# Kernel optimization log

Hardware: AMD Instinct MI355X
Metric: run time of the kernel (lower is better)

Reference implementation:

```python
import jax, jax.numpy as jnp
import numpy as np

D_CAT = 4096   # number of multinomial categories (input_dim)
HID = 256      # hidden_dim
B = 4096       # batch_size (eta is a (B, D_CAT-1) parameter)
INIT = 1e-3
LOG2PI = float(np.log(2.0 * np.pi))


def _helmert_basis(d):
    """Orthonormal ILR balance basis, shape (d-1, d): rows sum to 0, Psi @ Psi.T = I."""
    i = np.arange(1, d, dtype=np.float64)
    scale = np.sqrt(i / (i + 1.0))
    Psi = np.zeros((d - 1, d), dtype=np.float64)
    tri = np.tril(np.ones((d - 1, d - 1), dtype=np.float64))
    Psi[:, : d - 1] = tri * (scale / i)[:, None]
    Psi[np.arange(d - 1), np.arange(1, d)] = -scale
    return Psi.astype(np.float32)


def setup_inputs() -> dict:
    key = jax.random.key(0)
    k1, k2, k3, k4 = jax.random.split(key, 4)
    n = D_CAT - 1
    x = jax.random.randint(k1, (B, D_CAT), 0, 20).astype(jnp.float32)  # count data
    Psi = jnp.asarray(_helmert_basis(D_CAT))                            # (n, D)
    enc_W = jax.random.normal(k2, (HID, n), dtype=jnp.float32) * INIT   # encoder Linear weight
    dec_W = jax.random.normal(k3, (n, HID), dtype=jnp.float32) * INIT   # decoder Linear weight
    variational_logvars = jnp.zeros((HID,), jnp.float32)
    log_sigma_sq = jnp.float32(0.01)
    eta = jax.random.normal(k4, (B, n), dtype=jnp.float32) * INIT       # learned eta parameter
    return dict(x=x, Psi=Psi, enc_W=enc_W, dec_W=dec_W,
                variational_logvars=variational_logvars,
                log_sigma_sq=log_sigma_sq, eta=eta)


def reference(x, Psi, enc_W, dec_W, variational_logvars, log_sigma_sq, eta):
    # --- ILR transform of imputed counts: clr(log(x+1)) @ Psi^T ---
    logp = jnp.log(x + 1.0)                                   # imputer: x + 1
    clr = logp - logp.mean(-1, keepdims=True)                 # (B, D)
    hx = clr @ Psi.T                                          # (B, n)
    z_mean = hx @ enc_W.T                                     # (B, k)
    mu = z_mean @ dec_W.T                                     # (B, n)

    # --- MultivariateNormalFactorIdentity log_prob via Woodbury / det lemma ---
    # Sigma = var * I_n + W diag(Dv) W^T,  W = dec_W (n, k)
    Dv = jnp.exp(variational_logvars)                         # (k,)
    var = jnp.exp(log_sigma_sq)                               # scalar
    n = dec_W.shape[0]
    WtW = dec_W.T @ dec_W                                     # (k, k)
    M = jnp.diag(1.0 / Dv) + WtW / var                        # capacitance matrix (k, k)
    d = eta - mu                                              # (B, n)
    dW = d @ dec_W                                            # (B, k)
    sol = jnp.linalg.solve(M, dW.T).T                         # (B, k)
    quad = jnp.sum(d * d, -1) / var - jnp.sum(dW * sol, -1) / (var * var)
    _, logdetM = jnp.linalg.slogdet(M)
    logdet_sigma = n * log_sigma_sq + jnp.sum(variational_logvars) + logdetM
    logit_loss = jnp.mean(-0.5 * (n * LOG2PI + logdet_sigma + quad))

    # --- standard-normal prior on z_mean ---
    prior_loss = jnp.mean(-0.5 * z_mean * z_mean - 0.5 * LOG2PI)

    # --- Multinomial log-likelihood with logits = ilr_inv(eta) = eta @ Psi ---
    logits = eta @ Psi                                        # (B, D)
    logsm = jax.nn.log_softmax(logits, -1)
    ntot = x.sum(-1)
    mult = (jax.lax.lgamma(ntot + 1.0)
            - jnp.sum(jax.lax.lgamma(x + 1.0), -1)
            + jnp.sum(x * logsm, -1))
    mult_loss = jnp.mean(mult)

    return -(mult_loss + logit_loss + prior_loss)
```

## Files before the change

### kernel.cpp

```cpp
#include <hip/hip_runtime.h>
#include <math.h>

static constexpr int DC  = 4096;
static constexpr int NM1 = 4095;
static constexpr int HID = 256;
static constexpr int BB  = 4096;
static constexpr double LOG2PI_D = 1.8378770664093454835;

typedef __attribute__((ext_vector_type(8))) __bf16 bf16x8;
typedef __attribute__((ext_vector_type(4))) __bf16 bf16x4;
typedef __attribute__((ext_vector_type(2))) __bf16 bf16x2;
typedef __attribute__((ext_vector_type(4))) float  f32x4;

__device__ __forceinline__ void async16(const __bf16* g, __bf16* l) {
    __builtin_amdgcn_global_load_lds(
        (const __attribute__((address_space(1))) void*)g,
        (__attribute__((address_space(3))) void*)l, 16, 0, 0);
}

__global__ void k_scalars_coeffs(const float* __restrict__ lv, const float* __restrict__ lss,
                                 const float* __restrict__ Psi, float* __restrict__ Dv,
                                 float* __restrict__ scal, float* __restrict__ av,
                                 float* __restrict__ bv) {
    int t = threadIdx.x;
    if (blockIdx.x < 16) {
        int r = blockIdx.x * 256 + t;
        if (r < NM1) {
            av[r] = Psi[(size_t)r * DC];
            bv[r] = -Psi[(size_t)r * DC + r + 1];
        } else { av[r] = 0.f; bv[r] = 0.f; }
        return;
    }
    float v = lv[t];
    Dv[t] = expf(v);
    for (int o = 32; o > 0; o >>= 1) v += __shfl_down(v, o);
    __shared__ float red[4];
    if ((t & 63) == 0) red[t >> 6] = v;
    __syncthreads();
    if (t == 0) {
        scal[0] = expf(lss[0]);
        scal[1] = red[0] + red[1] + red[2] + red[3];
    }
}

__global__ __launch_bounds__(256) void k_mega(
    const float* __restrict__ x, const float* __restrict__ eta,
    const float* __restrict__ encW, const float* __restrict__ decW,
    const float* __restrict__ av, const float* __restrict__ bv,
    float* __restrict__ multv, float* __restrict__ eta2,
    __bf16* __restrict__ clrB, __bf16* __restrict__ etaB,
    __bf16* __restrict__ encPsiB, __bf16* __restrict__ decWT)
{
    __shared__ float smemf[4192];
    const int t = threadIdx.x;
    const int blk = blockIdx.x;
    const int lane = t & 63, w = t >> 6;

    if (blk < BB) {
        __bf16* xs   = (__bf16*)smemf;
        __bf16* es   = (__bf16*)(smemf + 2048);
        float* red   = smemf + 4096;
        float* wsumE = smemf + 4108;
        float* wsumX = smemf + 4112;
        float* lutL  = smemf + 4116;
        float* lutG  = smemf + 4148;
        const int b = blk;

        if (t < 32) { float f = (float)t + 1.f; lutL[t] = logf(f); lutG[t] = lgammaf(f); }
        const float4* x4 = (const float4*)(x + (size_t)b * DC);
        float4 xq[4];
        #pragma unroll
        for (int i = 0; i < 4; i++) xq[i] = x4[(i * 1024 + t * 4) >> 2];
        const float* erow = eta + (size_t)b * NM1;
        float ee[16];
        #pragma unroll
        for (int i = 0; i < 16; i++) { int j = i * 256 + t; ee[i] = (j < NM1) ? erow[j] : 0.f; }
        __syncthreads();

        float s = 0.f, slg = 0.f, slp = 0.f;
        #pragma unroll
        for (int i = 0; i < 4; i++) {
            int idx = i * 1024 + t * 4;
            float vv[4] = {xq[i].x, xq[i].y, xq[i].z, xq[i].w};
            bf16x4 xb;
            #pragma unroll
            for (int u = 0; u < 4; u++) {
                float vf = vv[u];
                int iv = (int)vf;
                float l, g;
                if (vf == (float)iv && iv >= 0 && iv < 32) { l = lutL[iv]; g = lutG[iv]; }
                else { l = logf(vf + 1.f); g = lgammaf(vf + 1.f); }
                s += vf; slg += g; slp += l;
                xb[u] = (__bf16)vf;
            }
            *(bf16x4*)&xs[idx] = xb;
        }
        float e2 = 0.f;
        #pragma unroll
        for (int i = 0; i < 16; i++) {
            int j = i * 256 + t;
            float e = ee[i];
            e2 += e * e;
            __bf16 eb = (__bf16)e;
            es[j] = eb;
            etaB[(size_t)b * DC + j] = eb;
        }
        for (int o = 32; o > 0; o >>= 1) {
            s += __shfl_down(s, o); slg += __shfl_down(slg, o); slp += __shfl_down(slp, o);
        }
        if (lane == 0) { red[0 + w] = s; red[4 + w] = slg; red[8 + w] = slp; }
        __syncthreads();

        const float ntotv  = red[0] + red[1] + red[2] + red[3];
        const float sumlgv = red[4] + red[5] + red[6] + red[7];
        const float m = (red[8] + red[9] + red[10] + red[11]) * (1.f / DC);

        #pragma unroll
        for (int i = 0; i < 4; i++) {
            int idx = i * 1024 + t * 4;
            bf16x4 xb = *(bf16x4*)&xs[idx];
            bf16x4 cb;
            #pragma unroll
            for (int u = 0; u < 4; u++) {
                float vf = (float)xb[u];
                int iv = (int)vf;
                float l = (iv >= 0 && iv < 32 && vf == (float)iv) ? lutL[iv] : logf(vf + 1.f);
                cb[u] = (__bf16)(l - m);
            }
            *(bf16x4*)(clrB + (size_t)b * DC + idx) = cb;
        }

        const int j0 = t * 16;
        float ev[16], xv[16], avc[16], bvc[16];
        {
            bf16x8 ea = *(const bf16x8*)(es + j0), eb8 = *(const bf16x8*)(es + j0 + 8);
            bf16x8 xa = *(const bf16x8*)(xs + j0), xb8 = *(const bf16x8*)(xs + j0 + 8);
            #pragma unroll
            for (int i = 0; i < 8; i++) {
                ev[i] = (float)ea[i]; ev[i + 8] = (float)eb8[i];
                xv[i] = (float)xa[i]; xv[i + 8] = (float)xb8[i];
            }
        }
        #pragma unroll
        for (int i = 0; i < 16; i += 4) {
            float4 a4 = *(const float4*)(av + j0 + i);
            avc[i] = a4.x; avc[i + 1] = a4.y; avc[i + 2] = a4.z; avc[i + 3] = a4.w;
            float4 b4 = *(const float4*)(bv + j0 + i);
            bvc[i] = b4.x; bvc[i + 1] = b4.y; bvc[i + 2] = b4.z; bvc[i + 3] = b4.w;
        }
        float localE = 0.f, localX = 0.f;
        #pragma unroll
        for (int i = 0; i < 16; i++) { localE += ev[i] * avc[i]; localX += xv[i]; }
        float incE = localE, incX = localX;
        #pragma unroll
        for (int o = 1; o < 64; o <<= 1) {
            float vE = __shfl_up(incE, o), vX = __shfl_up(incX, o);
            if (lane >= o) { incE += vE; incX += vX; }
        }
        if (lane == 63) { wsumE[w] = incE; wsumX[w] = incX; }
        float eprev = (t > 0) ? (float)es[j0 - 1] : 0.f;
        float bprev = (t > 0) ? bv[j0 - 1] : 0.f;
        float xnl   = (t < 255) ? (float)xs[j0 + 16] : 0.f;
        __syncthreads();

        float woffE = 0.f, woffX = 0.f;
        for (int i = 0; i < w; i++) { woffE += wsumE[i]; woffX += wsumX[i]; }
        const float U = wsumE[0] + wsumE[1] + wsumE[2] + wsumE[3];
        float runE = woffE + incE - localE;
        float Xrun = woffX + incX - localX;

        float se = 0.f, sx = 0.f;
        #pragma unroll
        for (int i = 0; i < 16; i++) {
            float Tj = U - runE;
            runE += ev[i] * avc[i];
            float pw = (i == 0) ? eprev * bprev : ev[i - 1] * bvc[i - 1];
            float l = Tj - pw;
            se += expf(l);
            Xrun += xv[i];
            float xn = (i < 15) ? xv[i + 1] : xnl;
            sx += ev[i] * (avc[i] * Xrun - bvc[i] * xn);
        }
        for (int o = 32; o > 0; o >>= 1) {
            se += __shfl_down(se, o); sx += __shfl_down(sx, o); e2 += __shfl_down(e2, o);
        }
        if (lane == 0) { red[0 + w] = se; red[4 + w] = sx; red[8 + w] = e2; }
        __syncthreads();
        if (t == 0) {
            float S1t = red[0] + red[1] + red[2] + red[3];
            float S2t = red[4] + red[5] + red[6] + red[7];
            float e2t = red[8] + red[9] + red[10] + red[11];
            double mult = (double)lgammaf(ntotv + 1.f) - (double)sumlgv
                        + (double)S2t - (double)ntotv * (double)logf(S1t);
            multv[b] = (float)mult;
            eta2[b]  = e2t;
        }
    } else if (blk < BB + HID) {
        __bf16* es   = (__bf16*)smemf;
        float* wsumE = smemf + 2048;
        const int h = blk - BB;
        const float* erow = encW + (size_t)h * NM1;
        float ee[16];
        #pragma unroll
        for (int i = 0; i < 16; i++) { int j = i * 256 + t; ee[i] = (j < NM1) ? erow[j] : 0.f; }
        #pragma unroll
        for (int i = 0; i < 16; i++) es[i * 256 + t] = (__bf16)ee[i];
        __syncthreads();
        const int j0 = t * 16;
        float ev[16], avc[16], bvc[16];
        {
            bf16x8 ea = *(const bf16x8*)(es + j0), eb8 = *(const bf16x8*)(es + j0 + 8);
            #pragma unroll
            for (int i = 0; i < 8; i++) { ev[i] = (float)ea[i]; ev[i + 8] = (float)eb8[i]; }
        }
        #pragma unroll
        for (int i = 0; i < 16; i += 4) {
            float4 a4 = *(const float4*)(av + j0 + i);
            avc[i] = a4.x; avc[i + 1] = a4.y; avc[i + 2] = a4.z; avc[i + 3] = a4.w;
            float4 b4 = *(const float4*)(bv + j0 + i);
            bvc[i] = b4.x; bvc[i + 1] = b4.y; bvc[i + 2] = b4.z; bvc[i + 3] = b4.w;
        }
        float localE = 0.f;
        #pragma unroll
        for (int i = 0; i < 16; i++) localE += ev[i] * avc[i];
        float incE = localE;
        #pragma unroll
        for (int o = 1; o < 64; o <<= 1) { float vE = __shfl_up(incE, o); if (lane >= o) incE += vE; }
        if (lane == 63) wsumE[w] = incE;
        float eprev = (t > 0) ? (float)es[j0 - 1] : 0.f;
        float bprev = (t > 0) ? bv[j0 - 1] : 0.f;
        __syncthreads();
        float woffE = 0.f;
        for (int i = 0; i < w; i++) woffE += wsumE[i];
        const float U = wsumE[0] + wsumE[1] + wsumE[2] + wsumE[3];
        float runE = woffE + incE - localE;
        bf16x8 o0, o1;
        #pragma unroll
        for (int i = 0; i < 16; i++) {
            float Tj = U - runE;
            runE += ev[i] * avc[i];
            float pw = (i == 0) ? eprev * bprev : ev[i - 1] * bvc[i - 1];
            float l = Tj - pw;
            if (i < 8) o0[i] = (__bf16)l; else o1[i - 8] = (__bf16)l;
        }
        *(bf16x8*)(encPsiB + (size_t)h * DC + j0)     = o0;
        *(bf16x8*)(encPsiB + (size_t)h * DC + j0 + 8) = o1;
    } else {
        float (*tp)[33] = (float(*)[33])smemf;
        int blk2 = blk - (BB + HID);
        int bx = blk2 & 7, by = blk2 >> 3;
        int tx = t & 31, ty = t >> 5;
        int r0 = by * 32, c0 = bx * 32;
        #pragma unroll
        for (int i = 0; i < 4; i++) {
            int r = r0 + ty + i * 8, c = c0 + tx;
            tp[ty + i * 8][tx] = (r < NM1 && c < HID) ? decW[(size_t)r * HID + c] : 0.f;
        }
        __syncthreads();
        #pragma unroll
        for (int i = 0; i < 4; i++) {
            int c = c0 + ty + i * 8, r = r0 + tx;
            decWT[(size_t)c * DC + r] = (__bf16)tp[tx][ty + i * 8];
        }
    }
}

__global__ __launch_bounds__(256) void mfma_combo(
    const __bf16* __restrict__ clrB, const __bf16* __restrict__ etaB,
    const __bf16* __restrict__ encPsiB, const __bf16* __restrict__ decWT,
    float* __restrict__ z_mean, float* __restrict__ etaW, float* __restrict__ WtW)
{
    __shared__ __bf16 As[64 * 32];
    __shared__ __bf16 Bs[256 * 32];
    const int tid = threadIdx.x;
    const int w = tid >> 6, lane = tid & 63;
    const int ln = lane & 15, q = lane >> 4;
    const int wm = w >> 1, wn = w & 1;
    const int bid = blockIdx.x;

    if (bid < 1024) {
        const int g = bid >> 9, r = bid & 511, sl = r >> 6, mt = r & 63;
        const __bf16* A  = g ? etaB  : clrB;
        const __bf16* Bt = g ? decWT : encPsiB;
        float* C = g ? etaW : z_mean;
        const int m0 = mt * 64, kb = sl * 512;
        f32x4 acc[2][8] = {};
        for (int k0 = kb; k0 < kb + 512; k0 += 32) {
            async16(A + (size_t)(m0 + (tid >> 2)) * DC + k0 + (tid & 3) * 8, As + tid * 8);
            #pragma unroll
            for (int j = 0; j < 4; j++) {
                int c = j * 256 + tid;
                async16(Bt + (size_t)(c >> 2) * DC + k0 + (c & 3) * 8, Bs + c * 8);
            }
            __syncthreads();
            bf16x8 af[2], bfr[8];
            #pragma unroll
            for (int i = 0; i < 2; i++) af[i]  = *(const bf16x8*)(As + (wm * 32 + i * 16 + ln) * 32 + q * 8);
            #pragma unroll
            for (int i = 0; i < 8; i++) bfr[i] = *(const bf16x8*)(Bs + (wn * 128 + i * 16 + ln) * 32 + q * 8);
            #pragma unroll
            for (int mi = 0; mi < 2; mi++)
                #pragma unroll
                for (int ni = 0; ni < 8; ni++)
                    acc[mi][ni] = __builtin_amdgcn_mfma_f32_16x16x32_bf16(af[mi], bfr[ni], acc[mi][ni], 0, 0, 0);
            __syncthreads();
        }
        #pragma unroll
        for (int mi = 0; mi < 2; mi++)
            #pragma unroll
            for (int rr = 0; rr < 4; rr++) {
                int m = m0 + wm * 32 + mi * 16 + q * 4 + rr;
                #pragma unroll
                for (int ni = 0; ni < 8; ni++) {
                    int n = wn * 128 + ni * 16 + ln;
                    atomicAdd(&C[(size_t)m * HID + n], acc[mi][ni][rr]);
                }
            }
    } else {
        const int w2 = bid - 1024;
        const int mn = w2 & 15, sl = w2 >> 4;
        const int m0 = (mn >> 2) * 64, n0 = (mn & 3) * 64, kb = sl * 512;
        f32x4 acc[2][2] = {};
        for (int k0 = kb; k0 < kb + 512; k0 += 32) {
            async16(decWT + (size_t)(m0 + (tid >> 2)) * DC + k0 + (tid & 3) * 8, As + tid * 8);
            async16(decWT + (size_t)(n0 + (tid >> 2)) * DC + k0 + (tid & 3) * 8, Bs + tid * 8);
            __syncthreads();
            bf16x8 af[2], bfr[2];
            #pragma unroll
            for (int i = 0; i < 2; i++) {
                af[i]  = *(const bf16x8*)(As + (wm * 32 + i * 16 + ln) * 32 + q * 8);
                bfr[i] = *(const bf16x8*)(Bs + (wn * 32 + i * 16 + ln) * 32 + q * 8);
            }
            #pragma unroll
            for (int mi = 0; mi < 2; mi++)
                #pragma unroll
                for (int ni = 0; ni < 2; ni++)
                    acc[mi][ni] = __builtin_amdgcn_mfma_f32_16x16x32_bf16(af[mi], bfr[ni], acc[mi][ni], 0, 0, 0);
            __syncthreads();
        }
        #pragma unroll
        for (int mi = 0; mi < 2; mi++)
            #pragma unroll
            for (int rr = 0; rr < 4; rr++) {
                int m = m0 + wm * 32 + mi * 16 + q * 4 + rr;
                #pragma unroll
                for (int ni = 0; ni < 2; ni++)
                    atomicAdd(&WtW[(size_t)m * HID + n0 + wn * 32 + ni * 16 + ln], acc[mi][ni][rr]);
            }
    }
}

__global__ __launch_bounds__(256) void k_cap(
    const float* __restrict__ WtW, const float* __restrict__ Dv,
    const float* __restrict__ scal, __bf16* __restrict__ WtWB,
    __bf16* __restrict__ MinvB, float* __restrict__ scal_out)
{
    __shared__ __bf16 As[64 * 32];
    __shared__ __bf16 Bs[64 * 32];
    __shared__ float dvs[HID];
    __shared__ float redc[8];
    const int tid = threadIdx.x;
    const int w = tid >> 6, lane = tid & 63;
    const int ln = lane & 15, q = lane >> 4;
    const int wm = w >> 1, wn = w & 1;
    const int m0 = (blockIdx.x >> 2) * 64, n0 = (blockIdx.x & 3) * 64;
    dvs[tid] = Dv[tid];
    __syncthreads();
    const float rv = 1.f / scal[0];
    f32x4 acc[2][2] = {};
    for (int k0 = 0; k0 < HID; k0 += 32) {
        {
            int row = tid >> 2, kc = tid & 3;
            const float* srcA = WtW + (size_t)(m0 + row) * HID + k0 + kc * 8;
            const float* srcB = WtW + (size_t)(n0 + row) * HID + k0 + kc * 8;
            float sA = dvs[m0 + row] * rv;
            bf16x8 a8, b8;
            #pragma unroll
            for (int u = 0; u < 8; u++) {
                a8[u] = (__bf16)(srcA[u] * sA);
                b8[u] = (__bf16)(srcB[u] * dvs[k0 + kc * 8 + u] * rv);
            }
            *(bf16x8*)(As + tid * 8) = a8;
            *(bf16x8*)(Bs + tid * 8) = b8;
        }
        __syncthreads();
        bf16x8 af[2], bfr[2];
        #pragma unroll
        for (int i = 0; i < 2; i++) {
            af[i]  = *(const bf16x8*)(As + (wm * 32 + i * 16 + ln) * 32 + q * 8);
            bfr[i] = *(const bf16x8*)(Bs + (wn * 32 + i * 16 + ln) * 32 + q * 8);
        }
        #pragma unroll
        for (int mi = 0; mi < 2; mi++)
            #pragma unroll
            for (int ni = 0; ni < 2; ni++)
                acc[mi][ni] = __builtin_amdgcn_mfma_f32_16x16x32_bf16(af[mi], bfr[ni], acc[mi][ni], 0, 0, 0);
        __syncthreads();
    }
    float t1p = 0.f, t2p = 0.f;
    #pragma unroll
    for (int mi = 0; mi < 2; mi++)
        #pragma unroll
        for (int rr = 0; rr < 4; rr++) {
            int m = m0 + wm * 32 + mi * 16 + q * 4 + rr;
            #pragma unroll
            for (int ni = 0; ni < 2; ni++) {
                int n = n0 + wn * 32 + ni * 16 + ln;
                float wmn = WtW[(size_t)m * HID + n];
                float Bmn = dvs[m] * wmn * rv;
                float Bnm = dvs[n] * wmn * rv;
                float mv = (((m == n) ? 1.f : 0.f) - Bmn + acc[mi][ni][rr]) * dvs[n];
                MinvB[(size_t)m * HID + n] = (__bf16)mv;
                WtWB[(size_t)m * HID + n] = (__bf16)wmn;
                t2p += Bmn * Bnm;
                if (m == n) t1p += Bmn;
            }
        }
    for (int o = 32; o > 0; o >>= 1) { t1p += __shfl_down(t1p, o); t2p += __shfl_down(t2p, o); }
    if (lane == 0) { redc[w] = t1p; redc[4 + w] = t2p; }
    __syncthreads();
    if (tid == 0) {
        atomicAdd(&scal_out[2], redc[0] + redc[1] + redc[2] + redc[3]);
        atomicAdd(&scal_out[3], redc[4] + redc[5] + redc[6] + redc[7]);
    }
}

__global__ __launch_bounds__(256) void mfma_quad(
    const float* __restrict__ z_mean, const float* __restrict__ etaW,
    const __bf16* __restrict__ WtWB, const __bf16* __restrict__ MinvB,
    float* __restrict__ r0a, float* __restrict__ r1a, float* __restrict__ r2a,
    float* __restrict__ r3a)
{
    __shared__ __bf16 As[16 * 32];
    __shared__ __bf16 Bs[256 * 32];
    __shared__ __bf16 dWs[16 * 264];
    const int tid = threadIdx.x;
    const int w = tid >> 6, lane = tid & 63;
    const int ln = lane & 15, q = lane >> 4;
    const int m0 = blockIdx.x * 16;

    f32x4 acc[4] = {};
    for (int k0 = 0; k0 < HID; k0 += 32) {
        {
            int row = tid >> 4, kc = tid & 15;
            float2 v = *(const float2*)(z_mean + (size_t)(m0 + row) * HID + k0 + kc * 2);
            bf16x2 b2 = {(__bf16)v.x, (__bf16)v.y};
            *(bf16x2*)(As + row * 32 + kc * 2) = b2;
        }
        #pragma unroll
        for (int j = 0; j < 4; j++) {
            int c = j * 256 + tid;
            async16(WtWB + (size_t)(c >> 2) * HID + k0 + (c & 3) * 8, Bs + c * 8);
        }
        __syncthreads();
        bf16x8 af = *(const bf16x8*)(As + ln * 32 + q * 8);
        #pragma unroll
        for (int ni = 0; ni < 4; ni++) {
            bf16x8 bfr = *(const bf16x8*)(Bs + (w * 64 + ni * 16 + ln) * 32 + q * 8);
            acc[ni] = __builtin_amdgcn_mfma_f32_16x16x32_bf16(af, bfr, acc[ni], 0, 0, 0);
        }
        __syncthreads();
    }
    #pragma unroll
    for (int rr = 0; rr < 4; rr++) {
        int lm = q * 4 + rr;
        int m = m0 + lm;
        float s0 = 0.f, s1 = 0.f, s3 = 0.f;
        #pragma unroll
        for (int ni = 0; ni < 4; ni++) {
            int n = w * 64 + ni * 16 + ln;
            float zv = z_mean[(size_t)m * HID + n];
            float ew = etaW[(size_t)m * HID + n];
            float dv = ew - acc[ni][rr];
            dWs[lm * 264 + n] = (__bf16)dv;
            s0 += ew * zv; s1 += dv * zv; s3 += zv * zv;
        }
        #pragma unroll
        for (int o = 1; o < 16; o <<= 1) {
            s0 += __shfl_xor(s0, o); s1 += __shfl_xor(s1, o); s3 += __shfl_xor(s3, o);
        }
        if (ln == 0) {
            atomicAdd(&r0a[m], s0); atomicAdd(&r1a[m], s1); atomicAdd(&r3a[m], s3);
        }
    }

    f32x4 acc2[4] = {};
    for (int k0 = 0; k0 < HID; k0 += 32) {
        #pragma unroll
        for (int j = 0; j < 4; j++) {
            int c = j * 256 + tid;
            async16(MinvB + (size_t)(c >> 2) * HID + k0 + (c & 3) * 8, Bs + c * 8);
        }
        __syncthreads();
        bf16x8 af = *(const bf16x8*)(dWs + ln * 264 + k0 + q * 8);
        #pragma unroll
        for (int ni = 0; ni < 4; ni++) {
            bf16x8 bfr = *(const bf16x8*)(Bs + (w * 64 + ni * 16 + ln) * 32 + q * 8);
            acc2[ni] = __builtin_amdgcn_mfma_f32_16x16x32_bf16(af, bfr, acc2[ni], 0, 0, 0);
        }
        __syncthreads();
    }
    #pragma unroll
    for (int rr = 0; rr < 4; rr++) {
        int lm = q * 4 + rr;
        int m = m0 + lm;
        float s2 = 0.f;
        #pragma unroll
        for (int ni = 0; ni < 4; ni++) {
            int n = w * 64 + ni * 16 + ln;
            s2 += (float)dWs[lm * 264 + n] * acc2[ni][rr];
        }
        #pragma unroll
        for (int o = 1; o < 16; o <<= 1) s2 += __shfl_xor(s2, o);
        if (ln == 0) atomicAdd(&r2a[m], s2);
    }
}

__global__ void k_final(const float* __restrict__ multv, const float* __restrict__ eta2,
                        const float* __restrict__ r0a, const float* __restrict__ r1a,
                        const float* __restrict__ r2a, const float* __restrict__ r3a,
                        const float* __restrict__ scal, const float* __restrict__ lss,
                        float* __restrict__ out) {
    int t = threadIdx.x;
    float var = scal[0];
    float rv = 1.f / var;
    double am = 0.0, aq = 0.0, az = 0.0;
    for (int b = t; b < BB; b += 256) {
        am += (double)multv[b];
        aq += (double)((eta2[b] - r0a[b] - r1a[b]) * rv - r2a[b] * rv * rv);
        az += (double)r3a[b];
    }
    for (int o = 32; o > 0; o >>= 1) {
        am += __shfl_down(am, o); aq += __shfl_down(aq, o); az += __shfl_down(az, o);
    }
    __shared__ double red[3][4];
    if ((t & 63) == 0) { int w = t >> 6; red[0][w] = am; red[1][w] = aq; red[2][w] = az; }
    __syncthreads();
    if (t == 0) {
        double mm = (red[0][0] + red[0][1] + red[0][2] + red[0][3]) / (double)BB;
        double mq = (red[1][0] + red[1][1] + red[1][2] + red[1][3]) / (double)BB;
        double mz = (red[2][0] + red[2][1] + red[2][2] + red[2][3]) / ((double)BB * (double)HID);
        double t1 = scal[2], t2 = scal[3];
        double logdetIB = t1 - t2 * 0.5;
        double sumlv = (double)scal[1];
        double logdetM = -sumlv + logdetIB;
        double logdet_sigma = (double)NM1 * (double)lss[0] + sumlv + logdetM;
        double logit_loss = -0.5 * ((double)NM1 * LOG2PI_D + logdet_sigma + mq);
        double prior_loss = -0.5 * mz - 0.5 * LOG2PI_D;
        out[0] = (float)(-(mm + logit_loss + prior_loss));
    }
}


extern "C" void kernel_launch(void* const* d_in, const int* in_sizes, int n_in,
                              void* d_out, int out_size, void* d_ws, size_t ws_size,
                              hipStream_t stream) {
    (void)in_sizes; (void)n_in; (void)out_size; (void)ws_size;
    const float* x    = (const float*)d_in[0];
    const float* Psi  = (const float*)d_in[1];
    const float* encW = (const float*)d_in[2];
    const float* decW = (const float*)d_in[3];
    const float* lv   = (const float*)d_in[4];
    const float* lss  = (const float*)d_in[5];
    const float* eta  = (const float*)d_in[6];
    float* out = (float*)d_out;

    float* wp = (float*)d_ws;
    float* z_mean = wp;
    float* etaW   = z_mean + (1 << 20);
    float* WtW    = etaW   + (1 << 20);
    float* r0a    = WtW    + 65536;
    float* r1a    = r0a    + 4096;
    float* r2a    = r1a    + 4096;
    float* r3a    = r2a    + 4096;
    float* scal   = r3a    + 4096;
    float* av     = scal   + 16;
    float* bv     = av     + 4096;
    float* multv  = bv     + 4096;
    float* eta2   = multv  + 4096;
    float* Dv     = eta2   + 4096;
    __bf16* clrB    = (__bf16*)(Dv + 256);
    __bf16* etaB    = clrB    + (1 << 24);
    __bf16* encPsiB = etaB    + (1 << 24);
    __bf16* decWT   = encPsiB + (1 << 20);
    __bf16* WtWB    = decWT   + (1 << 20);
    __bf16* MinvB   = WtWB    + 65536;

    hipMemsetAsync(z_mean, 0, (size_t)(2 * (1 << 20) + 65536 + 4 * 4096 + 16) * sizeof(float), stream);

    k_scalars_coeffs<<<17, 256, 0, stream>>>(lv, lss, Psi, Dv, scal, av, bv);

    k_mega<<<BB + HID + 1024, 256, 0, stream>>>(x, eta, encW, decW, av, bv,
                                                multv, eta2, clrB, etaB, encPsiB, decWT);

    mfma_combo<<<1152, 256, 0, stream>>>(clrB, etaB, encPsiB, decWT, z_mean, etaW, WtW);

    k_cap<<<16, 256, 0, stream>>>(WtW, Dv, scal, WtWB, MinvB, scal);

    mfma_quad<<<256, 256, 0, stream>>>(z_mean, etaW, WtWB, MinvB, r0a, r1a, r2a, r3a);

    k_final<<<1, 256, 0, stream>>>(multv, eta2, r0a, r1a, r2a, r3a, scal, lss, out);
}
```

Before: 321.8 us.

## Reschedule stages: move transpose to prep, WtW into mega, fuse capacitance into combo

The decW transpose moves into the prep kernel, so the WtW Gram GEMM can run as extra blocks inside the row-wise k_mega kernel. The capacitance-matrix kernel is merged into the main GEMM kernel as extra blocks, which removes one launch and one dependency stage. The main GEMM now uses a 64-wide K step with 1024-long K slices, halving the block count and the number of split-K atomic adds. Inside k_mega some loads are hoisted earlier and the order of reductions and syncs is changed to overlap memory latency. The cost is fewer blocks per GEMM, which lowers parallelism, and more LDS per block in the combo kernel.

Measured after the change: 297.8 us. 7.5% less time.

```diff
diff --git a/kernel.cpp b/kernel.cpp
--- a/kernel.cpp
+++ b/kernel.cpp
@@ -18,38 +18,57 @@
         (__attribute__((address_space(3))) void*)l, 16, 0, 0);
 }
 
-__global__ void k_scalars_coeffs(const float* __restrict__ lv, const float* __restrict__ lss,
-                                 const float* __restrict__ Psi, float* __restrict__ Dv,
-                                 float* __restrict__ scal, float* __restrict__ av,
-                                 float* __restrict__ bv) {
-    int t = threadIdx.x;
-    if (blockIdx.x < 16) {
-        int r = blockIdx.x * 256 + t;
+__global__ __launch_bounds__(256) void k_pre(
+    const float* __restrict__ decW, const float* __restrict__ Psi,
+    const float* __restrict__ lv, const float* __restrict__ lss,
+    __bf16* __restrict__ decWT, float* __restrict__ av, float* __restrict__ bv,
+    float* __restrict__ Dv, float* __restrict__ scal)
+{
+    __shared__ float tp[32][33];
+    const int t = threadIdx.x;
+    const int blk = blockIdx.x;
+    if (blk < 1024) {
+        int bx = blk & 7, by = blk >> 3;
+        int tx = t & 31, ty = t >> 5;
+        int r0 = by * 32, c0 = bx * 32;
+        #pragma unroll
+        for (int i = 0; i < 4; i++) {
+            int r = r0 + ty + i * 8, c = c0 + tx;
+            tp[ty + i * 8][tx] = (r < NM1 && c < HID) ? decW[(size_t)r * HID + c] : 0.f;
+        }
+        __syncthreads();
+        #pragma unroll
+        for (int i = 0; i < 4; i++) {
+            int c = c0 + ty + i * 8, r = r0 + tx;
+            decWT[(size_t)c * DC + r] = (__bf16)tp[tx][ty + i * 8];
+        }
+    } else if (blk < 1040) {
+        int r = (blk - 1024) * 256 + t;
         if (r < NM1) {
             av[r] = Psi[(size_t)r * DC];
             bv[r] = -Psi[(size_t)r * DC + r + 1];
         } else { av[r] = 0.f; bv[r] = 0.f; }
-        return;
-    }
-    float v = lv[t];
-    Dv[t] = expf(v);
-    for (int o = 32; o > 0; o >>= 1) v += __shfl_down(v, o);
-    __shared__ float red[4];
-    if ((t & 63) == 0) red[t >> 6] = v;
-    __syncthreads();
-    if (t == 0) {
-        scal[0] = expf(lss[0]);
-        scal[1] = red[0] + red[1] + red[2] + red[3];
+    } else {
+        float v = lv[t];
+        Dv[t] = expf(v);
+        for (int o = 32; o > 0; o >>= 1) v += __shfl_down(v, o);
+        __shared__ float red[4];
+        if ((t & 63) == 0) red[t >> 6] = v;
+        __syncthreads();
+        if (t == 0) {
+            scal[0] = expf(lss[0]);
+            scal[1] = red[0] + red[1] + red[2] + red[3];
+        }
     }
 }
 
 __global__ __launch_bounds__(256) void k_mega(
     const float* __restrict__ x, const float* __restrict__ eta,
-    const float* __restrict__ encW, const float* __restrict__ decW,
+    const float* __restrict__ encW, const __bf16* __restrict__ decWT,
     const float* __restrict__ av, const float* __restrict__ bv,
     float* __restrict__ multv, float* __restrict__ eta2,
     __bf16* __restrict__ clrB, __bf16* __restrict__ etaB,
-    __bf16* __restrict__ encPsiB, __bf16* __restrict__ decWT)
+    __bf16* __restrict__ encPsiB, float* __restrict__ WtW)
 {
     __shared__ float smemf[4192];
     const int t = threadIdx.x;
@@ -66,16 +85,26 @@
         float* lutG  = smemf + 4148;
         const int b = blk;
 
-        if (t < 32) { float f = (float)t + 1.f; lutL[t] = logf(f); lutG[t] = lgammaf(f); }
         const float4* x4 = (const float4*)(x + (size_t)b * DC);
         float4 xq[4];
         #pragma unroll
         for (int i = 0; i < 4; i++) xq[i] = x4[(i * 1024 + t * 4) >> 2];
+        if (t < 32) { float f = (float)t + 1.f; lutL[t] = logf(f); lutG[t] = lgammaf(f); }
+        __syncthreads();
+
         const float* erow = eta + (size_t)b * NM1;
         float ee[16];
         #pragma unroll
         for (int i = 0; i < 16; i++) { int j = i * 256 + t; ee[i] = (j < NM1) ? erow[j] : 0.f; }
-        __syncthreads();
+        const int j0 = t * 16;
+        float avc[16], bvc[16];
+        #pragma unroll
+        for (int i = 0; i < 16; i += 4) {
+            float4 a4 = *(const float4*)(av + j0 + i);
+            avc[i] = a4.x; avc[i + 1] = a4.y; avc[i + 2] = a4.z; avc[i + 3] = a4.w;
+            float4 b4 = *(const float4*)(bv + j0 + i);
+            bvc[i] = b4.x; bvc[i + 1] = b4.y; bvc[i + 2] = b4.z; bvc[i + 3] = b4.w;
+        }
 
         float s = 0.f, slg = 0.f, slp = 0.f;
         #pragma unroll
@@ -95,6 +124,30 @@
             }
             *(bf16x4*)&xs[idx] = xb;
         }
+        for (int o = 32; o > 0; o >>= 1) {
+            s += __shfl_down(s, o); slg += __shfl_down(slg, o); slp += __shfl_down(slp, o);
+        }
+        if (lane == 0) { red[0 + w] = s; red[4 + w] = slg; red[8 + w] = slp; }
+        __syncthreads();
+
+        const float ntotv  = red[0] + red[1] + red[2] + red[3];
+        const float sumlgv = red[4] + red[5] + red[6] + red[7];
+        const float m = (red[8] + red[9] + red[10] + red[11]) * (1.f / DC);
+
+        #pragma unroll
+        for (int i = 0; i < 4; i++) {
+            int idx = i * 1024 + t * 4;
+            bf16x4 xb = *(bf16x4*)&xs[idx];
+            bf16x4 cb;
+            #pragma unroll
+            for (int u = 0; u < 4; u++) {
+                float vf = (float)xb[u];
+                int iv = (int)vf;
+                float l = (iv >= 0 && iv < 32 && vf == (float)iv) ? lutL[iv] : logf(vf + 1.f);
+                cb[u] = (__bf16)(l - m);
+            }
+            *(bf16x4*)(clrB + (size_t)b * DC + idx) = cb;
+        }
         float e2 = 0.f;
         #pragma unroll
         for (int i = 0; i < 16; i++) {
@@ -105,33 +158,9 @@
             es[j] = eb;
             etaB[(size_t)b * DC + j] = eb;
         }
-        for (int o = 32; o > 0; o >>= 1) {
-            s += __shfl_down(s, o); slg += __shfl_down(slg, o); slp += __shfl_down(slp, o);
-        }
-        if (lane == 0) { red[0 + w] = s; red[4 + w] = slg; red[8 + w] = slp; }
-        __syncthreads();
-
-        const float ntotv  = red[0] + red[1] + red[2] + red[3];
-        const float sumlgv = red[4] + red[5] + red[6] + red[7];
-        const float m = (red[8] + red[9] + red[10] + red[11]) * (1.f / DC);
-
-        #pragma unroll
-        for (int i = 0; i < 4; i++) {
-            int idx = i * 1024 + t * 4;
-            bf16x4 xb = *(bf16x4*)&xs[idx];
-            bf16x4 cb;
-            #pragma unroll
-            for (int u = 0; u < 4; u++) {
-                float vf = (float)xb[u];
-                int iv = (int)vf;
-                float l = (iv >= 0 && iv < 32 && vf == (float)iv) ? lutL[iv] : logf(vf + 1.f);
-                cb[u] = (__bf16)(l - m);
-            }
-            *(bf16x4*)(clrB + (size_t)b * DC + idx) = cb;
-        }
-
-        const int j0 = t * 16;
-        float ev[16], xv[16], avc[16], bvc[16];
+        __syncthreads();
+
+        float ev[16], xv[16];
         {
             bf16x8 ea = *(const bf16x8*)(es + j0), eb8 = *(const bf16x8*)(es + j0 + 8);
             bf16x8 xa = *(const bf16x8*)(xs + j0), xb8 = *(const bf16x8*)(xs + j0 + 8);
@@ -140,13 +169,6 @@
                 ev[i] = (float)ea[i]; ev[i + 8] = (float)eb8[i];
                 xv[i] = (float)xa[i]; xv[i + 8] = (float)xb8[i];
             }
-        }
-        #pragma unroll
-        for (int i = 0; i < 16; i += 4) {
-            float4 a4 = *(const float4*)(av + j0 + i);
-            avc[i] = a4.x; avc[i + 1] = a4.y; avc[i + 2] = a4.z; avc[i + 3] = a4.w;
-            float4 b4 = *(const float4*)(bv + j0 + i);
-            bvc[i] = b4.x; bvc[i + 1] = b4.y; bvc[i + 2] = b4.z; bvc[i + 3] = b4.w;
         }
         float localE = 0.f, localX = 0.f;
         #pragma unroll
@@ -203,22 +225,23 @@
         float ee[16];
         #pragma unroll
         for (int i = 0; i < 16; i++) { int j = i * 256 + t; ee[i] = (j < NM1) ? erow[j] : 0.f; }
-        #pragma unroll
-        for (int i = 0; i < 16; i++) es[i * 256 + t] = (__bf16)ee[i];
-        __syncthreads();
         const int j0 = t * 16;
-        float ev[16], avc[16], bvc[16];
-        {
-            bf16x8 ea = *(const bf16x8*)(es + j0), eb8 = *(const bf16x8*)(es + j0 + 8);
-            #pragma unroll
-            for (int i = 0; i < 8; i++) { ev[i] = (float)ea[i]; ev[i + 8] = (float)eb8[i]; }
-        }
+        float avc[16], bvc[16];
         #pragma unroll
         for (int i = 0; i < 16; i += 4) {
             float4 a4 = *(const float4*)(av + j0 + i);
             avc[i] = a4.x; avc[i + 1] = a4.y; avc[i + 2] = a4.z; avc[i + 3] = a4.w;
             float4 b4 = *(const float4*)(bv + j0 + i);
             bvc[i] = b4.x; bvc[i + 1] = b4.y; bvc[i + 2] = b4.z; bvc[i + 3] = b4.w;
+        }
+        #pragma unroll
+        for (int i = 0; i < 16; i++) es[i * 256 + t] = (__bf16)ee[i];
+        __syncthreads();
+        float ev[16];
+        {
+            bf16x8 ea = *(const bf16x8*)(es + j0), eb8 = *(const bf16x8*)(es + j0 + 8);
+            #pragma unroll
+            for (int i = 0; i < 8; i++) { ev[i] = (float)ea[i]; ev[i + 8] = (float)eb8[i]; }
         }
         float localE = 0.f;
         #pragma unroll
@@ -246,63 +269,93 @@
         *(bf16x8*)(encPsiB + (size_t)h * DC + j0)     = o0;
         *(bf16x8*)(encPsiB + (size_t)h * DC + j0 + 8) = o1;
     } else {
-        float (*tp)[33] = (float(*)[33])smemf;
-        int blk2 = blk - (BB + HID);
-        int bx = blk2 & 7, by = blk2 >> 3;
-        int tx = t & 31, ty = t >> 5;
-        int r0 = by * 32, c0 = bx * 32;
-        #pragma unroll
-        for (int i = 0; i < 4; i++) {
-            int r = r0 + ty + i * 8, c = c0 + tx;
-            tp[ty + i * 8][tx] = (r < NM1 && c < HID) ? decW[(size_t)r * HID + c] : 0.f;
-        }
-        __syncthreads();
-        #pragma unroll
-        for (int i = 0; i < 4; i++) {
-            int c = c0 + ty + i * 8, r = r0 + tx;
-            decWT[(size_t)c * DC + r] = (__bf16)tp[tx][ty + i * 8];
-        }
+        __bf16* As = (__bf16*)smemf;
+        __bf16* Bs = (__bf16*)(smemf + 1024);
+        const int w2 = blk - (BB + HID);
+        const int mn = w2 & 15, sl = w2 >> 4;
+        const int m0 = (mn >> 2) * 64, n0 = (mn & 3) * 64, kb = sl * 1024;
+        const int ln = lane & 15, q = lane >> 4;
+        const int wm = w >> 1, wn = w & 1;
+        f32x4 acc[2][2] = {};
+        for (int k0 = kb; k0 < kb + 1024; k0 += 32) {
+            async16(decWT + (size_t)(m0 + (t >> 2)) * DC + k0 + (t & 3) * 8, As + t * 8);
+            async16(decWT + (size_t)(n0 + (t >> 2)) * DC + k0 + (t & 3) * 8, Bs + t * 8);
+            __syncthreads();
+            bf16x8 af[2], bfr[2];
+            #pragma unroll
+            for (int i = 0; i < 2; i++) {
+                af[i]  = *(const bf16x8*)(As + (wm * 32 + i * 16 + ln) * 32 + q * 8);
+                bfr[i] = *(const bf16x8*)(Bs + (wn * 32 + i * 16 + ln) * 32 + q * 8);
+            }
+            #pragma unroll
+            for (int mi = 0; mi < 2; mi++)
+                #pragma unroll
+                for (int ni = 0; ni < 2; ni++)
+                    acc[mi][ni] = __builtin_amdgcn_mfma_f32_16x16x32_bf16(af[mi], bfr[ni], acc[mi][ni], 0, 0, 0);
+            __syncthreads();
+        }
+        #pragma unroll
+        for (int mi = 0; mi < 2; mi++)
+            #pragma unroll
+            for (int rr = 0; rr < 4; rr++) {
+                int m = m0 + wm * 32 + mi * 16 + q * 4 + rr;
+                #pragma unroll
+                for (int ni = 0; ni < 2; ni++)
+                    atomicAdd(&WtW[(size_t)m * HID + n0 + wn * 32 + ni * 16 + ln], acc[mi][ni][rr]);
+            }
     }
 }
 
-__global__ __launch_bounds__(256) void mfma_combo(
+__global__ __launch_bounds__(256) void k_combo2(
     const __bf16* __restrict__ clrB, const __bf16* __restrict__ etaB,
     const __bf16* __restrict__ encPsiB, const __bf16* __restrict__ decWT,
-    float* __restrict__ z_mean, float* __restrict__ etaW, float* __restrict__ WtW)
+    float* __restrict__ z_mean, float* __restrict__ etaW,
+    const float* __restrict__ WtW, const float* __restrict__ Dv,
+    const float* __restrict__ scal, __bf16* __restrict__ WtWB,
+    __bf16* __restrict__ MinvB, float* __restrict__ scal_out)
 {
-    __shared__ __bf16 As[64 * 32];
-    __shared__ __bf16 Bs[256 * 32];
+    __shared__ __bf16 As[64 * 64];
+    __shared__ __bf16 Bs[256 * 64];
     const int tid = threadIdx.x;
     const int w = tid >> 6, lane = tid & 63;
     const int ln = lane & 15, q = lane >> 4;
     const int wm = w >> 1, wn = w & 1;
     const int bid = blockIdx.x;
 
-    if (bid < 1024) {
-        const int g = bid >> 9, r = bid & 511, sl = r >> 6, mt = r & 63;
+    if (bid < 512) {
+        const int g = bid >> 8, r = bid & 255, sl = r >> 6, mt = r & 63;
         const __bf16* A  = g ? etaB  : clrB;
         const __bf16* Bt = g ? decWT : encPsiB;
         float* C = g ? etaW : z_mean;
-        const int m0 = mt * 64, kb = sl * 512;
+        const int m0 = mt * 64, kb = sl * 1024;
         f32x4 acc[2][8] = {};
-        for (int k0 = kb; k0 < kb + 512; k0 += 32) {
-            async16(A + (size_t)(m0 + (tid >> 2)) * DC + k0 + (tid & 3) * 8, As + tid * 8);
-            #pragma unroll
-            for (int j = 0; j < 4; j++) {
+        for (int k0 = kb; k0 < kb + 1024; k0 += 64) {
+            #pragma unroll
+            for (int j = 0; j < 2; j++) {
                 int c = j * 256 + tid;
-                async16(Bt + (size_t)(c >> 2) * DC + k0 + (c & 3) * 8, Bs + c * 8);
+                async16(A + (size_t)(m0 + (c >> 3)) * DC + k0 + (c & 7) * 8, As + c * 8);
+            }
+            #pragma unroll
+            for (int j = 0; j < 8; j++) {
+                int c = j * 256 + tid;
+                async16(Bt + (size_t)(c >> 3) * DC + k0 + (c & 7) * 8, Bs + c * 8);
             }
             __syncthreads();
-            bf16x8 af[2], bfr[8];
-            #pragma unroll
-            for (int i = 0; i < 2; i++) af[i]  = *(const bf16x8*)(As + (wm * 32 + i * 16 + ln) * 32 + q * 8);
-            #pragma unroll
-            for (int i = 0; i < 8; i++) bfr[i] = *(const bf16x8*)(Bs + (wn * 128 + i * 16 + ln) * 32 + q * 8);
-            #pragma unroll
-            for (int mi = 0; mi < 2; mi++)
-                #pragma unroll
-                for (int ni = 0; ni < 8; ni++)
-                    acc[mi][ni] = __builtin_amdgcn_mfma_f32_16x16x32_bf16(af[mi], bfr[ni], acc[mi][ni], 0, 0, 0);
+            #pragma unroll
+            for (int jj = 0; jj < 2; jj++) {
+                bf16x8 af[2], bfr[8];
+                #pragma unroll
+                for (int i = 0; i < 2; i++)
+                    af[i]  = *(const bf16x8*)(As + (wm * 32 + i * 16 + ln) * 64 + jj * 32 + q * 8);
+                #pragma unroll
+                for (int i = 0; i < 8; i++)
+                    bfr[i] = *(const bf16x8*)(Bs + (wn * 128 + i * 16 + ln) * 64 + jj * 32 + q * 8);
+                #pragma unroll
+                for (int mi = 0; mi < 2; mi++)
+                    #pragma unroll
+                    for (int ni = 0; ni < 8; ni++)
+                        acc[mi][ni] = __builtin_amdgcn_mfma_f32_16x16x32_bf16(af[mi], bfr[ni], acc[mi][ni], 0, 0, 0);
+            }
             __syncthreads();
         }
         #pragma unroll
@@ -317,13 +370,29 @@
                 }
             }
     } else {
-        const int w2 = bid - 1024;
-        const int mn = w2 & 15, sl = w2 >> 4;
-        const int m0 = (mn >> 2) * 64, n0 = (mn & 3) * 64, kb = sl * 512;
+        __shared__ float dvs[HID];
+        __shared__ float redc[8];
+        const int w2 = bid - 512;
+        const int m0 = (w2 >> 2) * 64, n0 = (w2 & 3) * 64;
+        dvs[tid] = Dv[tid];
+        __syncthreads();
+        const float rv = 1.f / scal[0];
         f32x4 acc[2][2] = {};
-        for (int k0 = kb; k0 < kb + 512; k0 += 32) {
-            async16(decWT + (size_t)(m0 + (tid >> 2)) * DC + k0 + (tid & 3) * 8, As + tid * 8);
-            async16(decWT + (size_t)(n0 + (tid >> 2)) * DC + k0 + (tid & 3) * 8, Bs + tid * 8);
+        for (int k0 = 0; k0 < HID; k0 += 32) {
+            {
+                int row = tid >> 2, kc = tid & 3;
+                const float* srcA = WtW + (size_t)(m0 + row) * HID + k0 + kc * 8;
+                const float* srcB = WtW + (size_t)(n0 + row) * HID + k0 + kc * 8;
+                float sA = dvs[m0 + row] * rv;
+                bf16x8 a8, b8;
+                #pragma unroll
+                for (int u = 0; u < 8; u++) {
+                    a8[u] = (__bf16)(srcA[u] * sA);
+                    b8[u] = (__bf16)(srcB[u] * dvs[k0 + kc * 8 + u] * rv);
+                }
+                *(bf16x8*)(As + tid * 8) = a8;
+                *(bf16x8*)(Bs + tid * 8) = b8;
+            }
             __syncthreads();
             bf16x8 af[2], bfr[2];
             #pragma unroll
@@ -338,90 +407,32 @@
                     acc[mi][ni] = __builtin_amdgcn_mfma_f32_16x16x32_bf16(af[mi], bfr[ni], acc[mi][ni], 0, 0, 0);
             __syncthreads();
         }
+        float t1p = 0.f, t2p = 0.f;
         #pragma unroll
         for (int mi = 0; mi < 2; mi++)
             #pragma unroll
             for (int rr = 0; rr < 4; rr++) {
                 int m = m0 + wm * 32 + mi * 16 + q * 4 + rr;
                 #pragma unroll
-                for (int ni = 0; ni < 2; ni++)
-                    atomicAdd(&WtW[(size_t)m * HID + n0 + wn * 32 + ni * 16 + ln], acc[mi][ni][rr]);
-            }
-    }
-}
-
-__global__ __launch_bounds__(256) void k_cap(
-    const float* __restrict__ WtW, const float* __restrict__ Dv,
-    const float* __restrict__ scal, __bf16* __restrict__ WtWB,
-    __bf16* __restrict__ MinvB, float* __restrict__ scal_out)
-{
-    __shared__ __bf16 As[64 * 32];
-    __shared__ __bf16 Bs[64 * 32];
-    __shared__ float dvs[HID];
-    __shared__ float redc[8];
-    const int tid = threadIdx.x;
-    const int w = tid >> 6, lane = tid & 63;
-    const int ln = lane & 15, q = lane >> 4;
-    const int wm = w >> 1, wn = w & 1;
-    const int m0 = (blockIdx.x >> 2) * 64, n0 = (blockIdx.x & 3) * 64;
-    dvs[tid] = Dv[tid];
-    __syncthreads();
-    const float rv = 1.f / scal[0];
-    f32x4 acc[2][2] = {};
-    for (int k0 = 0; k0 < HID; k0 += 32) {
-        {
-            int row = tid >> 2, kc = tid & 3;
-            const float* srcA = WtW + (size_t)(m0 + row) * HID + k0 + kc * 8;
-            const float* srcB = WtW + (size_t)(n0 + row) * HID + k0 + kc * 8;
-            float sA = dvs[m0 + row] * rv;
-            bf16x8 a8, b8;
-            #pragma unroll
-            for (int u = 0; u < 8; u++) {
-                a8[u] = (__bf16)(srcA[u] * sA);
-                b8[u] = (__bf16)(srcB[u] * dvs[k0 + kc * 8 + u] * rv);
-            }
-            *(bf16x8*)(As + tid * 8) = a8;
-            *(bf16x8*)(Bs + tid * 8) = b8;
-        }
-        __syncthreads();
-        bf16x8 af[2], bfr[2];
-        #pragma unroll
-        for (int i = 0; i < 2; i++) {
-            af[i]  = *(const bf16x8*)(As + (wm * 32 + i * 16 + ln) * 32 + q * 8);
-            bfr[i] = *(const bf16x8*)(Bs + (wn * 32 + i * 16 + ln) * 32 + q * 8);
-        }
-        #pragma unroll
-        for (int mi = 0; mi < 2; mi++)
-            #pragma unroll
-            for (int ni = 0; ni < 2; ni++)
-                acc[mi][ni] = __builtin_amdgcn_mfma_f32_16x16x32_bf16(af[mi], bfr[ni], acc[mi][ni], 0, 0, 0);
-        __syncthreads();
-    }
-    float t1p = 0.f, t2p = 0.f;
-    #pragma unroll
-    for (int mi = 0; mi < 2; mi++)
-        #pragma unroll
-        for (int rr = 0; rr < 4; rr++) {
-            int m = m0 + wm * 32 + mi * 16 + q * 4 + rr;
-            #pragma unroll
-            for (int ni = 0; ni < 2; ni++) {
-                int n = n0 + wn * 32 + ni * 16 + ln;
-                float wmn = WtW[(size_t)m * HID + n];
-                float Bmn = dvs[m] * wmn * rv;
-                float Bnm = dvs[n] * wmn * rv;
-                float mv = (((m == n) ? 1.f : 0.f) - Bmn + acc[mi][ni][rr]) * dvs[n];
-                MinvB[(size_t)m * HID + n] = (__bf16)mv;
-                WtWB[(size_t)m * HID + n] = (__bf16)wmn;
-                t2p += Bmn * Bnm;
-                if (m == n) t1p += Bmn;
-            }
-        }
-    for (int o = 32; o > 0; o >>= 1) { t1p += __shfl_down(t1p, o); t2p += __shfl_down(t2p, o); }
-    if (lane == 0) { redc[w] = t1p; redc[4 + w] = t2p; }
-    __syncthreads();
-    if (tid == 0) {
-        atomicAdd(&scal_out[2], redc[0] + redc[1] + redc[2] + redc[3]);
-        atomicAdd(&scal_out[3], redc[4] + redc[5] + redc[6] + redc[7]);
+                for (int ni = 0; ni < 2; ni++) {
+                    int n = n0 + wn * 32 + ni * 16 + ln;
+                    float wmn = WtW[(size_t)m * HID + n];
+                    float Bmn = dvs[m] * wmn * rv;
+                    float Bnm = dvs[n] * wmn * rv;
+                    float mv = (((m == n) ? 1.f : 0.f) - Bmn + acc[mi][ni][rr]) * dvs[n];
+                    MinvB[(size_t)m * HID + n] = (__bf16)mv;
+                    WtWB[(size_t)m * HID + n] = (__bf16)wmn;
+                    t2p += Bmn * Bnm;
+                    if (m == n) t1p += Bmn;
+                }
+            }
+        for (int o = 32; o > 0; o >>= 1) { t1p += __shfl_down(t1p, o); t2p += __shfl_down(t2p, o); }
+        if (lane == 0) { redc[w] = t1p; redc[4 + w] = t2p; }
+        __syncthreads();
+        if (tid == 0) {
+            atomicAdd(&scal_out[2], redc[0] + redc[1] + redc[2] + redc[3]);
+            atomicAdd(&scal_out[3], redc[4] + redc[5] + redc[6] + redc[7]);
+        }
     }
 }
 
@@ -588,14 +599,13 @@
 
     hipMemsetAsync(z_mean, 0, (size_t)(2 * (1 << 20) + 65536 + 4 * 4096 + 16) * sizeof(float), stream);
 
-    k_scalars_coeffs<<<17, 256, 0, stream>>>(lv, lss, Psi, Dv, scal, av, bv);
-
-    k_mega<<<BB + HID + 1024, 256, 0, stream>>>(x, eta, encW, decW, av, bv,
-                                                multv, eta2, clrB, etaB, encPsiB, decWT);
-
-    mfma_combo<<<1152, 256, 0, stream>>>(clrB, etaB, encPsiB, decWT, z_mean, etaW, WtW);
-
-    k_cap<<<16, 256, 0, stream>>>(WtW, Dv, scal, WtWB, MinvB, scal);
+    k_pre<<<1041, 256, 0, stream>>>(decW, Psi, lv, lss, decWT, av, bv, Dv, scal);
+
+    k_mega<<<BB + HID + 64, 256, 0, stream>>>(x, eta, encW, decWT, av, bv,
+                                              multv, eta2, clrB, etaB, encPsiB, WtW);
+
+    k_combo2<<<528, 256, 0, stream>>>(clrB, etaB, encPsiB, decWT, z_mean, etaW,
+                                      WtW, Dv, scal, WtWB, MinvB, scal);
 
     mfma_quad<<<256, 256, 0, stream>>>(z_mean, etaW, WtWB, MinvB, r0a, r1a, r2a, r3a);
 
```
